# Performance work log

Hardware: AMD Instinct MI355X
Metric: run time of the kernel (lower is better)

## Reference

```python
import jax, jax.numpy as jnp
import numpy as np

SCALE = 64 ** (-0.5)


def setup_inputs() -> dict:
    key = jax.random.key(0)
    ks = jax.random.split(key, 6)
    B, C, D, N = 2, 1024, 64, 128
    w_std = C ** (-0.5)
    return {
        "lidar": jax.random.normal(ks[0], (B, C, D, N), dtype=jnp.float32),
        "cam": jax.random.normal(ks[1], (B, C, D, N), dtype=jnp.float32),
        "Wq": jax.random.normal(ks[2], (C, C), dtype=jnp.float32) * w_std,
        "Wk": jax.random.normal(ks[3], (C, C), dtype=jnp.float32) * w_std,
        "Wv": jax.random.normal(ks[4], (C, C), dtype=jnp.float32) * w_std,
        "Wo": jax.random.normal(ks[5], (C, C), dtype=jnp.float32) * w_std,
    }


def _proj(W, x):
    # 1x1 Conv1d over flattened (D*N) positions == channel matmul, bias=False
    return jnp.einsum('oc,bcdn->bodn', W, x)


def reference(lidar, cam, Wq, Wk, Wv, Wo):
    q = _proj(Wq, lidar)  # [B, C, D, Ni]
    k = _proj(Wk, cam)    # [B, C, D, Nj]
    v = _proj(Wv, cam)    # [B, C, D, Nj]
    # contract over D (head-dim-like axis); scores per (batch, channel)
    dots = jnp.einsum('bhdi,bhdj->bhij', q, k) * SCALE  # [B, C, Ni, Nj]
    att = jax.nn.softmax(dots, axis=-1)
    # einsum 'a b i c,a b j c->a b j i': contract over cam positions
    out = jnp.einsum('bhic,bhjc->bhji', att, v)  # [B, C, D, Ni]
    out = jax.nn.gelu(_proj(Wo, out), approximate=False)
    return out
```

## Files before the change

kernel.cpp:

```cpp
#include <hip/hip_runtime.h>
#include <math.h>

#define CH  1024
#define PPB 8192

typedef __attribute__((ext_vector_type(8))) short short8;
typedef __attribute__((ext_vector_type(4))) float f32x4;

__device__ __forceinline__ ushort f2bf(float x) {
    uint u = __float_as_uint(x);
    return (ushort)((u + 0x7FFFu + ((u >> 16) & 1u)) >> 16);
}
__device__ __forceinline__ float bf2f(ushort u) {
    return __uint_as_float(((uint)u) << 16);
}
__device__ __forceinline__ void gload16(const void* g, const void* l) {
    __builtin_amdgcn_global_load_lds((const __attribute__((address_space(1))) void*)g,
                                     (__attribute__((address_space(3))) void*)l, 16, 0, 0);
}

__global__ __launch_bounds__(256) void prep(const float* __restrict__ lidar,
                                            const float* __restrict__ cam,
                                            const float* __restrict__ Wq,
                                            const float* __restrict__ Wk,
                                            const float* __restrict__ Wv,
                                            const float* __restrict__ Wo,
                                            ushort* __restrict__ wdst,
                                            ushort* __restrict__ lidT,
                                            ushort* __restrict__ camT)
{
    __shared__ float T[64][65];
    const int blk = blockIdx.x;
    const int tid = threadIdx.x;

    if (blk < 2048) {
        const int y = blk >> 9;
        const int x = blk & 511;
        const float* w = (y == 0) ? Wq : (y == 1) ? Wk : (y == 2) ? Wv : Wo;
        ushort* o = wdst + (size_t)y * (1u << 20);
        const int idx = (x * 256 + tid) * 8;
        const float4 v0 = *(const float4*)(w + idx);
        const float4 v1 = *(const float4*)(w + idx + 4);
        ushort4 o0, o1;
        o0.x = f2bf(v0.x); o0.y = f2bf(v0.y); o0.z = f2bf(v0.z); o0.w = f2bf(v0.w);
        o1.x = f2bf(v1.x); o1.y = f2bf(v1.y); o1.z = f2bf(v1.z); o1.w = f2bf(v1.w);
        *(ushort4*)(o + idx)     = o0;
        *(ushort4*)(o + idx + 4) = o1;
        return;
    }

    const int t = blk - 2048;
    const bool isLid = (t < 4096);
    const int tt = isLid ? t : t - 4096;
    const float* in = isLid ? lidar : cam;
    ushort* out = isLid ? lidT : camT;

    const int p0 = (tt & 127) * 64;
    const int c0 = ((tt >> 7) & 15) * 64;
    const int b  = tt >> 11;
    const int rc = tid >> 4;
    const int rp = (tid & 15) * 4;

    #pragma unroll
    for (int pass = 0; pass < 4; ++pass) {
        const int c = pass * 16 + rc;
        const size_t base = ((size_t)(b * CH + c0 + c)) * PPB + p0 + rp;
        const float4 v = *(const float4*)(in + base);
        T[c][rp] = v.x; T[c][rp + 1] = v.y; T[c][rp + 2] = v.z; T[c][rp + 3] = v.w;
    }
    __syncthreads();
    #pragma unroll
    for (int pass = 0; pass < 4; ++pass) {
        const int p = pass * 16 + rc;
        ushort4 o;
        o.x = f2bf(T[rp + 0][p]); o.y = f2bf(T[rp + 1][p]);
        o.z = f2bf(T[rp + 2][p]); o.w = f2bf(T[rp + 3][p]);
        *(ushort4*)(out + ((size_t)(b * PPB + p0 + p)) * CH + c0 + rp) = o;
    }
}

__global__ __launch_bounds__(256) void transpose_ao(const ushort* __restrict__ in_,
                                                    ushort* __restrict__ out)
{
    __shared__ float T[64][65];
    const int p0 = blockIdx.x * 64;
    const int c0 = blockIdx.y * 64;
    const int b  = blockIdx.z;
    const int t  = threadIdx.x;
    const int rc = t >> 4;
    const int rp = (t & 15) * 4;

    #pragma unroll
    for (int pass = 0; pass < 4; ++pass) {
        const int c = pass * 16 + rc;
        const size_t base = ((size_t)(b * CH + c0 + c)) * PPB + p0 + rp;
        const ushort4 v = *(const ushort4*)(in_ + base);
        T[c][rp]     = bf2f(v.x); T[c][rp + 1] = bf2f(v.y);
        T[c][rp + 2] = bf2f(v.z); T[c][rp + 3] = bf2f(v.w);
    }
    __syncthreads();
    #pragma unroll
    for (int pass = 0; pass < 4; ++pass) {
        const int p = pass * 16 + rc;
        const int prow = p * 128 + blockIdx.x;
        ushort4 o;
        o.x = f2bf(T[rp + 0][p]); o.y = f2bf(T[rp + 1][p]);
        o.z = f2bf(T[rp + 2][p]); o.w = f2bf(T[rp + 3][p]);
        *(ushort4*)(out + ((size_t)(b * PPB + prow)) * CH + c0 + rp) = o;
    }
}

template <int IS_WO>
__global__ __launch_bounds__(512, 2) void gemm256(const ushort* __restrict__ W3,
                                                  const ushort* __restrict__ lidT,
                                                  const ushort* __restrict__ camT,
                                                  void* __restrict__ outp)
{
    __shared__ __align__(16) ushort sh[65536];
    char* shb = (char*)sh;

    const int bid = blockIdx.x;
    int g, bm, bn;
    if (IS_WO) {
        const int sid = (bid & 7) * 32 + (bid >> 3);
        g = 3; bm = sid & 3; bn = sid >> 2;
    } else {
        const int sid = (bid & 7) * 96 + (bid >> 3);
        g = sid >> 8; const int r = sid & 255; bm = r & 3; bn = r >> 2;
    }
    const int m0  = bm * 256;
    const int b   = bn >> 5;
    const int nn0 = (bn & 31) * 4;
    const int n0  = bn * 256;
    const ushort* A  = W3 + (size_t)g * (1u << 20);
    const ushort* Bt = (g == 0) ? lidT : camT;
    const bool remap = (!IS_WO) && (g < 2);

    const int tid = threadIdx.x;
    const int w   = tid >> 6;
    const int l   = tid & 63;
    const int wr  = w >> 2;
    const int wc  = w & 3;
    const int hi  = l >> 4;
    const int fr  = l & 15;

    auto stageA = [&](int buf, int kt, int half) {
        const int k0 = kt * 64;
        #pragma unroll
        for (int ld = 0; ld < 2; ++ld) {
            const int c  = w * 2 + ld;
            const int rt = half * 128 + c * 8 + (l >> 3);
            const int kc = ((l & 7) ^ (rt & 7)) << 3;
            gload16(A + (size_t)(m0 + rt) * CH + k0 + kc,
                    &shb[buf * 32768 + half * 16384 + c * 1024]);
        }
    };
    auto stageB = [&](int buf, int kt, int half) {
        const int k0 = kt * 64;
        #pragma unroll
        for (int ld = 0; ld < 2; ++ld) {
            const int c  = w * 2 + ld;
            const int rt = half * 128 + c * 8 + (l >> 3);
            const int kc = ((l & 7) ^ (rt & 7)) << 3;
            size_t brow;
            if (remap) brow = (size_t)b * PPB + (size_t)(rt & 63) * 128 + nn0 + (rt >> 6);
            else       brow = (size_t)(n0 + rt);
            gload16(Bt + brow * CH + k0 + kc,
                    &shb[65536 + buf * 32768 + half * 16384 + c * 1024]);
        }
    };

    f32x4 acc[8][4];
    #pragma unroll
    for (int i = 0; i < 8; ++i)
        #pragma unroll
        for (int j = 0; j < 4; ++j) acc[i][j] = (f32x4)(0.0f);

    stageA(0, 0, 0); stageA(0, 0, 1); stageB(0, 0, 0); stageB(0, 0, 1);

    for (int kt = 0; kt < 16; ++kt) {
        const int buf = kt & 1, nxt = buf ^ 1;
        if (kt < 15) {
            stageA(nxt, kt + 1, 0);
            __builtin_amdgcn_sched_barrier(0);
            asm volatile("s_waitcnt vmcnt(2)" ::: "memory");
        } else {
            __builtin_amdgcn_sched_barrier(0);
            asm volatile("s_waitcnt vmcnt(0)" ::: "memory");
        }
        __builtin_amdgcn_s_barrier();
        __builtin_amdgcn_sched_barrier(0);
        const int Ab = buf * 32768, Bb = 65536 + buf * 32768;

        short8 aq[4][2], bq[2][2];
        auto LDA = [&](int mh) {
            #pragma unroll
            for (int fm = 0; fm < 4; ++fm) {
                const int row = wr * 128 + (mh * 4 + fm) * 16 + fr;
                #pragma unroll
                for (int kk = 0; kk < 2; ++kk)
                    aq[fm][kk] = *(const short8*)&shb[Ab + row * 128 +
                        ((((kk << 2) + hi) ^ (row & 7)) << 4)];
            }
        };
        auto LDB = [&](int nh) {
            #pragma unroll
            for (int fn = 0; fn < 2; ++fn) {
                const int row = wc * 64 + (nh * 2 + fn) * 16 + fr;
                #pragma unroll
                for (int kk = 0; kk < 2; ++kk)
                    bq[fn][kk] = *(const short8*)&shb[Bb + row * 128 +
                        ((((kk << 2) + hi) ^ (row & 7)) << 4)];
            }
        };
        auto MF = [&](int mh, int nh) {
            __builtin_amdgcn_s_setprio(1);
            #pragma unroll
            for (int kk = 0; kk < 2; ++kk)
                #pragma unroll
                for (int fm = 0; fm < 4; ++fm)
                    #pragma unroll
                    for (int fn = 0; fn < 2; ++fn)
                        acc[mh * 4 + fm][nh * 2 + fn] =
                            __builtin_amdgcn_mfma_f32_16x16x32_bf16(
                                aq[fm][kk], bq[fn][kk],
                                acc[mh * 4 + fm][nh * 2 + fn], 0, 0, 0);
            __builtin_amdgcn_s_setprio(0);
        };

        LDA(0); LDB(0);              MF(0, 0);
        if (kt < 15) stageA(nxt, kt + 1, 1);
        LDB(1);                      MF(0, 1);
        if (kt < 15) stageB(nxt, kt + 1, 0);
        LDA(1);                      MF(1, 1);
        if (kt < 15) stageB(nxt, kt + 1, 1);
        LDB(0);                      MF(1, 0);

        __builtin_amdgcn_sched_barrier(0);
        asm volatile("s_waitcnt lgkmcnt(0)" ::: "memory");
        __builtin_amdgcn_sched_barrier(0);
        __builtin_amdgcn_s_barrier();
    }

    #pragma unroll
    for (int fm = 0; fm < 8; ++fm)
        #pragma unroll
        for (int fn = 0; fn < 4; ++fn)
            #pragma unroll
            for (int r = 0; r < 4; ++r) {
                const int m = m0 + wr * 128 + fm * 16 + hi * 4 + r;
                const int s = (bn & 31) * 256 + wc * 64 + fn * 16 + fr;
                const float vv = acc[fm][fn][r];
                const size_t off = (size_t)b * CH * PPB + (size_t)m * PPB + s;
                if (IS_WO) {
                    ((float*)outp)[off] = 0.5f * vv * (1.0f + erff(vv * 0.70710678118654752f));
                } else {
                    ((ushort*)outp)[(size_t)g * ((size_t)16 << 20) + off] = f2bf(vv);
                }
            }
}

__global__ __launch_bounds__(256, 2) void attn_mfma(const ushort* __restrict__ qt,
                                                    const ushort* __restrict__ kt,
                                                    const ushort* __restrict__ vn,
                                                    ushort* __restrict__ ot)
{
    __shared__ ushort Qs[8192];
    __shared__ ushort Ks[8192];
    __shared__ ushort Vs[8192];
    __shared__ ushort Ps[16384];

    const int bh  = blockIdx.x;
    const int tid = threadIdx.x;
    const int w   = tid >> 6;
    const int l   = tid & 63;
    const int hi  = l >> 4;
    const int fr  = l & 15;
    const size_t base = (size_t)bh * 8192;

    {
        const int lr = l >> 3, lb = l & 7;
        const int vr = l >> 4, vbk = l & 15;
        #pragma unroll
        for (int q = 0; q < 4; ++q) {
            const int ch = w * 4 + q;
            const int i  = ch * 8 + lr;
            gload16(qt + base + i * 64 + ((lb ^ (i & 7)) << 3), &Qs[ch * 512]);
            gload16(kt + base + i * 64 + ((lb ^ (i & 7)) << 3), &Ks[ch * 512]);
            const int d  = ch * 4 + vr;
            gload16(vn + base + d * 128 + ((vbk ^ (d & 15)) << 3), &Vs[ch * 512]);
        }
    }
    __syncthreads();

    const int i0w = w * 32;
    f32x4 accS[2][8];
    #pragma unroll
    for (int a = 0; a < 2; ++a)
        #pragma unroll
        for (int bjj = 0; bjj < 8; ++bjj) accS[a][bjj] = (f32x4)(0.0f);

    #pragma unroll
    for (int kk = 0; kk < 2; ++kk) {
        const int blk = kk * 4 + hi;
        short8 aq[2];
        #pragma unroll
        for (int fm = 0; fm < 2; ++fm) {
            const int i = i0w + fm * 16 + fr;
            aq[fm] = *(const short8*)&Qs[i * 64 + ((blk ^ (i & 7)) << 3)];
        }
        #pragma unroll
        for (int fn = 0; fn < 8; ++fn) {
            const int j = fn * 16 + fr;
            const short8 bk = *(const short8*)&Ks[j * 64 + ((blk ^ (j & 7)) << 3)];
            #pragma unroll
            for (int fm = 0; fm < 2; ++fm)
                accS[fm][fn] = __builtin_amdgcn_mfma_f32_16x16x32_bf16(
                    aq[fm], bk, accS[fm][fn], 0, 0, 0);
        }
    }

    const float CS = 0.125f * 1.44269504088896341f;
    #pragma unroll
    for (int fm = 0; fm < 2; ++fm) {
        #pragma unroll
        for (int r = 0; r < 4; ++r) {
            float mx = accS[fm][0][r];
            #pragma unroll
            for (int fn = 1; fn < 8; ++fn) mx = fmaxf(mx, accS[fm][fn][r]);
            #pragma unroll
            for (int msk = 1; msk <= 8; msk <<= 1) mx = fmaxf(mx, __shfl_xor(mx, msk, 64));
            float e[8], sum = 0.f;
            #pragma unroll
            for (int fn = 0; fn < 8; ++fn) {
                e[fn] = exp2f((accS[fm][fn][r] - mx) * CS);
                sum += e[fn];
            }
            #pragma unroll
            for (int msk = 1; msk <= 8; msk <<= 1) sum += __shfl_xor(sum, msk, 64);
            const float is = 1.0f / sum;
            const int i = i0w + fm * 16 + hi * 4 + r;
            #pragma unroll
            for (int fn = 0; fn < 8; ++fn) {
                const int j = fn * 16 + fr;
                Ps[i * 128 + (((j >> 3) ^ (i & 15)) << 3) + (j & 7)] = f2bf(e[fn] * is);
            }
        }
    }

    f32x4 accO[2][4];
    #pragma unroll
    for (int a = 0; a < 2; ++a)
        #pragma unroll
        for (int bjj = 0; bjj < 4; ++bjj) accO[a][bjj] = (f32x4)(0.0f);

    #pragma unroll
    for (int ks2 = 0; ks2 < 4; ++ks2) {
        const int blk = ks2 * 4 + hi;
        short8 ap[2];
        #pragma unroll
        for (int fm = 0; fm < 2; ++fm) {
            const int i = i0w + fm * 16 + fr;
            ap[fm] = *(const short8*)&Ps[i * 128 + ((blk ^ (i & 15)) << 3)];
        }
        #pragma unroll
        for (int fn2 = 0; fn2 < 4; ++fn2) {
            const int d = fn2 * 16 + fr;
            const short8 bv = *(const short8*)&Vs[d * 128 + ((blk ^ (d & 15)) << 3)];
            #pragma unroll
            for (int fm = 0; fm < 2; ++fm)
                accO[fm][fn2] = __builtin_amdgcn_mfma_f32_16x16x32_bf16(
                    ap[fm], bv, accO[fm][fn2], 0, 0, 0);
        }
    }

    #pragma unroll
    for (int fm = 0; fm < 2; ++fm)
        #pragma unroll
        for (int fn2 = 0; fn2 < 4; ++fn2)
            #pragma unroll
            for (int r = 0; r < 4; ++r) {
                const int i = i0w + fm * 16 + hi * 4 + r;
                const int d = fn2 * 16 + fr;
                ot[base + i * 64 + d] = f2bf(accO[fm][fn2][r]);
            }
}

extern "C" void kernel_launch(void* const* d_in, const int* in_sizes, int n_in,
                              void* d_out, int out_size, void* d_ws, size_t ws_size,
                              hipStream_t stream)
{
    const float* lidar = (const float*)d_in[0];
    const float* cam   = (const float*)d_in[1];
    const float* Wq    = (const float*)d_in[2];
    const float* Wk    = (const float*)d_in[3];
    const float* Wv    = (const float*)d_in[4];
    const float* Wo    = (const float*)d_in[5];

    ushort* ws = (ushort*)d_ws;
    const size_t M1 = (size_t)1 << 20;
    const size_t TT = (size_t)16 << 20;
    ushort* lidT = ws + 4 * M1;
    ushort* camT = lidT + TT;
    ushort* qb   = camT + TT;
    ushort* aoT  = lidT;

    prep<<<dim3(10240), dim3(256), 0, stream>>>(lidar, cam, Wq, Wk, Wv, Wo, ws, lidT, camT);

    gemm256<0><<<dim3(768), dim3(512), 0, stream>>>(ws, lidT, camT, qb);

    attn_mfma<<<dim3(2048), dim3(256), 0, stream>>>(qb, qb + TT, qb + 2 * TT, qb);

    transpose_ao<<<dim3(128, 16, 2), dim3(256), 0, stream>>>(qb, aoT);

    gemm256<1><<<dim3(256), dim3(512), 0, stream>>>(ws, aoT, aoT, (float*)d_out);
}
```

Measured before the change: 259.9 us.

## Issue all next-tile global loads upfront and barrier after each MFMA phase

Moves all stageA/stageB prefetches for the next K tile to the start of each iteration, instead of interleaving them between MFMA phases, and waits with vmcnt(8). Each of the four LDS-read and MFMA phases now waits for lgkmcnt(0) before its MFMAs and ends with a workgroup barrier. This is meant to simplify the schedule and keep warps in lockstep, but it adds four barriers per K-step and removes the overlap of LDS reads with MFMA. The vmcnt(8) threshold may also no longer wait for the current buffer correctly.

```diff
diff --git a/kernel.cpp b/kernel.cpp
--- a/kernel.cpp
+++ b/kernel.cpp
@@ -181,9 +181,10 @@
     for (int kt = 0; kt < 16; ++kt) {
         const int buf = kt & 1, nxt = buf ^ 1;
         if (kt < 15) {
-            stageA(nxt, kt + 1, 0);
+            stageA(nxt, kt + 1, 0); stageA(nxt, kt + 1, 1);
+            stageB(nxt, kt + 1, 0); stageB(nxt, kt + 1, 1);
             __builtin_amdgcn_sched_barrier(0);
-            asm volatile("s_waitcnt vmcnt(2)" ::: "memory");
+            asm volatile("s_waitcnt vmcnt(8)" ::: "memory");
         } else {
             __builtin_amdgcn_sched_barrier(0);
             asm volatile("s_waitcnt vmcnt(0)" ::: "memory");
@@ -227,28 +228,44 @@
                                 acc[mh * 4 + fm][nh * 2 + fn], 0, 0, 0);
             __builtin_amdgcn_s_setprio(0);
         };
-
-        LDA(0); LDB(0);              MF(0, 0);
-        if (kt < 15) stageA(nxt, kt + 1, 1);
-        LDB(1);                      MF(0, 1);
-        if (kt < 15) stageB(nxt, kt + 1, 0);
-        LDA(1);                      MF(1, 1);
-        if (kt < 15) stageB(nxt, kt + 1, 1);
-        LDB(0);                      MF(1, 0);
-
+        auto PHASE_END = [&]() {
+            __builtin_amdgcn_sched_barrier(0);
+            asm volatile("s_waitcnt lgkmcnt(0)" ::: "memory");
+            __builtin_amdgcn_sched_barrier(0);
+            __builtin_amdgcn_s_barrier();
+            __builtin_amdgcn_sched_barrier(0);
+        };
+
+        LDA(0); LDB(0);
         __builtin_amdgcn_sched_barrier(0);
         asm volatile("s_waitcnt lgkmcnt(0)" ::: "memory");
         __builtin_amdgcn_sched_barrier(0);
-        __builtin_amdgcn_s_barrier();
-    }
-
+        MF(0, 0); PHASE_END();
+        LDB(1);
+        __builtin_amdgcn_sched_barrier(0);
+        asm volatile("s_waitcnt lgkmcnt(0)" ::: "memory");
+        __builtin_amdgcn_sched_barrier(0);
+        MF(0, 1); PHASE_END();
+        LDA(1);
+        __builtin_amdgcn_sched_barrier(0);
+        asm volatile("s_waitcnt lgkmcnt(0)" ::: "memory");
+        __builtin_amdgcn_sched_barrier(0);
+        MF(1, 1); PHASE_END();
+        LDB(0);
+        __builtin_amdgcn_sched_barrier(0);
+        asm volatile("s_waitcnt lgkmcnt(0)" ::: "memory");
+        __builtin_amdgcn_sched_barrier(0);
+        MF(1, 0); PHASE_END();
+    }
+
+    const int rq = hi;
     #pragma unroll
     for (int fm = 0; fm < 8; ++fm)
         #pragma unroll
         for (int fn = 0; fn < 4; ++fn)
             #pragma unroll
             for (int r = 0; r < 4; ++r) {
-                const int m = m0 + wr * 128 + fm * 16 + hi * 4 + r;
+                const int m = m0 + wr * 128 + fm * 16 + rq * 4 + r;
                 const int s = (bn & 31) * 256 + wc * 64 + fn * 16 + fr;
                 const float vv = acc[fm][fn][r];
                 const size_t off = (size_t)b * CH * PPB + (size_t)m * PPB + s;
```

Result: slower. 273.7 us (+5.3%).
